# Kernel optimization log

Measured on AMD Instinct MI355X. Metric: run time of the kernel, lower is better.

Reference implementation:

```python
import jax, jax.numpy as jnp
import numpy as np

TAU = 2.0      # membrane time constant
V_TH = 1.0     # spike threshold (v_reset = 0, hard reset)
T_STEPS = 4    # num_steps

@jax.custom_vjp
def heaviside_atan(x):
    # forward: Heaviside; backward: spikingjelly ATan surrogate (alpha=2)
    return (x >= 0.0).astype(x.dtype)

def _h_fwd(x):
    return heaviside_atan(x), x

def _h_bwd(x, g):
    alpha = 2.0
    return (g * (alpha / 2.0) / (1.0 + (jnp.pi / 2.0 * alpha * x) ** 2),)

heaviside_atan.defvjp(_h_fwd, _h_bwd)

def lif_multistep(x_seq):
    # spikingjelly LIFNode, step_mode='m', decay_input=True, v_reset=0, detach_reset=True
    def step(v, x):
        v = v + (x - v) / TAU                      # charge
        s = heaviside_atan(v - V_TH)               # fire (surrogate grad)
        v = v * (1.0 - jax.lax.stop_gradient(s))   # hard reset, detached spike
        return v, s
    v0 = jnp.zeros_like(x_seq[0])
    _, spikes = jax.lax.scan(step, v0, x_seq)
    return spikes

def setup_inputs() -> dict:
    key = jax.random.key(0)
    k0, k1, k2 = jax.random.split(key, 3)
    B, L, C, D, NL = 16, 512, 128, 1024, 2
    inputs = jax.random.normal(k0, (B, L, C), jnp.float32)
    enc_W = jax.random.normal(k1, (C, D), jnp.float32) / np.sqrt(C).astype(np.float32)
    enc_b = jnp.zeros((D,), jnp.float32)
    W_cells = jax.random.normal(k2, (NL, D, D), jnp.float32) / np.sqrt(D).astype(np.float32)
    b_cells = jnp.zeros((NL, D), jnp.float32)
    return {"inputs": inputs, "enc_W": enc_W, "enc_b": enc_b,
            "W_cells": W_cells, "b_cells": b_cells}

def reference(inputs, enc_W, enc_b, W_cells, b_cells):
    # temporal spike encoder: repeat input over T steps, LIF-encode to spikes
    x = jnp.swapaxes(inputs, 1, 2)                       # [B, C, L]
    x = jnp.broadcast_to(x[None], (T_STEPS,) + x.shape)  # [T, B, C, L]
    h = lif_multistep(x)
    h = jnp.swapaxes(h, -2, -1)                          # [T, B, L, C]
    # encoder linear + init LIF
    h = lif_multistep(h @ enc_W + enc_b)                 # [T, B, L, D]
    # stacked SpikeRNNCells: Linear(D,D) -> multistep LIF
    for i in range(W_cells.shape[0]):
        h = lif_multistep(h @ W_cells[i] + b_cells[i])
    out = h.mean(0)                                      # [B, L, D]
    return out, out.mean(axis=1)                         # ([B,L,D], [B,D])
```

## Files before the change

### kernel.cpp

```cpp
#include <hip/hip_runtime.h>
#include <hip/hip_bf16.h>
#include <stdint.h>

#define TSTEPS 4

typedef __bf16 bf16_t;
typedef __attribute__((ext_vector_type(8))) __bf16 bf16x8;
typedef __attribute__((ext_vector_type(16))) float f32x16;
typedef __attribute__((ext_vector_type(4))) unsigned short ushort4v;

union frag_u { bf16x8 v; uint32_t d[4]; unsigned short u[8]; };

#define WT_VM2_LG0  0x072
#define WT_VM2      0xF72
#define WT_LG0      0xC07F
#define WT_VM0_LG0  0x070


__global__ void spike_encode_i8(const float* __restrict__ x,
                                uint4* __restrict__ s1)
{
    const int C = 128;
    int tid = blockIdx.x * blockDim.x + threadIdx.x;
    int row = tid & 31;
    int kb  = (tid >> 5) & 7;
    int m_blk = tid >> 8;
    int m = m_blk * 32 + row;
    const float* px = x + (size_t)m * C + kb * 16;
    float xv[16];
#pragma unroll
    for (int j = 0; j < 16; j += 4) {
        float4 t4 = *(const float4*)(px + j);
        xv[j] = t4.x; xv[j+1] = t4.y; xv[j+2] = t4.z; xv[j+3] = t4.w;
    }
    float v[16];
#pragma unroll
    for (int j = 0; j < 16; ++j) v[j] = 0.0f;
#pragma unroll
    for (int t = 0; t < TSTEPS; ++t) {
        uint32_t dw[4] = {0u, 0u, 0u, 0u};
#pragma unroll
        for (int j = 0; j < 16; ++j) {
            float vv = __fadd_rn(v[j], __fmul_rn(__fsub_rn(xv[j], v[j]), 0.5f));
            bool sp = (vv >= 1.0f);
            dw[j >> 2] |= sp ? (0x3Fu << ((j & 3) * 8)) : 0u;
            v[j] = sp ? 0.0f : vv;
        }
        uint4 o; o.x = dw[0]; o.y = dw[1]; o.z = dw[2]; o.w = dw[3];
        s1[((size_t)(m_blk * 8 + kb) * 4 + t) * 32 + row] = o;
    }
}

__global__ void split_transpose_all(const float* __restrict__ enc_W,
                                    const float* __restrict__ W_cells,
                                    bf16_t* __restrict__ W1h, bf16_t* __restrict__ W1l,
                                    bf16_t* __restrict__ W2h, bf16_t* __restrict__ W2l,
                                    bf16_t* __restrict__ W3h, bf16_t* __restrict__ W3l)
{
    const int N = 1024;
    const float* W;
    bf16_t *hi, *lo;
    int K;
    if (blockIdx.z == 0) {
        if (blockIdx.x >= 4) return;
        W = enc_W; hi = W1h; lo = W1l; K = 128;
    } else if (blockIdx.z == 1) {
        W = W_cells; hi = W2h; lo = W2l; K = 1024;
    } else {
        W = W_cells + (size_t)1024 * 1024; hi = W3h; lo = W3l; K = 1024;
    }
    const int NKB = K >> 4;
    __shared__ float tile[32][33];
    int k0 = blockIdx.x * 32, n0 = blockIdx.y * 32;
    int tx = threadIdx.x & 31, ty = threadIdx.x >> 5;
    for (int kk = ty; kk < 32; kk += 8)
        tile[kk][tx] = W[(size_t)(k0 + kk) * N + n0 + tx];
    __syncthreads();

    const int nn = tx;
    const int oc = ty;
    const int o2 = oc & 3;
    const bool isLo = (oc >> 2) != 0;
    const int kblk = (k0 >> 4) + (o2 >> 1);
    const int lane_in_packet = nn + 32 * (o2 & 1);

    frag_u f;
#pragma unroll
    for (int j = 0; j < 8; ++j) {
        float wv = tile[o2 * 8 + j][nn];
        bf16_t h = (bf16_t)wv;
        bf16_t l = (bf16_t)(wv - (float)h);
        f.v[j] = isLo ? (bf16_t)(2.0f * (float)l)
                      : (bf16_t)(2.0f * (float)h);
    }
    bf16_t* dst = (isLo ? lo : hi)
        + ((size_t)((n0 + nn) >> 5) * NKB + kblk) * 512 + lane_in_packet * 8;
    *(bf16x8*)dst = f.v;
}

template <int K, bool LAST>
__global__ __launch_bounds__(256, 4)
void gemm_lif_mfma(const uint8_t* __restrict__ Abytes,
                   const bf16_t* __restrict__ Bh,
                   const bf16_t* __restrict__ Bl,
                   const float* __restrict__ bias,
                   uint8_t* __restrict__ Sbytes,
                   float* __restrict__ Out,
                   int M, int N)
{
    constexpr int NKB = K >> 4;
    __shared__ __align__(16) uint8_t ldsR[4][8192];
    __shared__ __align__(8) unsigned short sh[4][256];

    const int tid = threadIdx.x;
    const int lane = tid & 63;
    const int wid = tid >> 6;
    const int l31 = lane & 31;
    const int half = lane >> 5;

    const int bid = blockIdx.x;
    const int xcd = bid & 7;
    const int j   = bid >> 3;
    const int nh   = j >> 7;
    const int r    = j & 127;
    const int mloc = r >> 3;
    const int n_t  = nh * 8 + (r & 7);
    const int m_t  = xcd * 16 + mloc;

    const int m0 = m_t * 64, n0 = n_t * 64;
    const int wave_m = (wid & 1) * 32;
    const int wave_n = (wid >> 1) * 32;
    const int m_blk = (m0 + wave_m) >> 5;

    const uint8_t* src0;
    const uint8_t* src1;
    int sstride, d0off, d1off;
    if (wid < 2) {
        const uint8_t* base = Abytes + ((size_t)(m0 >> 5) + wid) * NKB * 2048;
        src0 = base + (lane << 4);
        src1 = base + 1024 + (lane << 4);
        sstride = 2048;
        d0off = wid * 2048;
        d1off = d0off + 1024;
    } else {
        const int nl = wid - 2;
        src0 = (const uint8_t*)(Bh + ((size_t)(n0 >> 5) + nl) * NKB * 512)
               + (lane << 4);
        src1 = (const uint8_t*)(Bl + ((size_t)(n0 >> 5) + nl) * NKB * 512)
               + (lane << 4);
        sstride = 1024;
        d0off = 4096 + nl * 2048;
        d1off = d0off + 1024;
    }
    uint8_t* ringBase = &ldsR[0][0];

    const int aRdOff = (wid & 1) * 2048 + l31 * 16 + half * 8;
    const int bRdOff = 4096 + ((wid >> 1) << 11) + (lane << 4);

    f32x16 acc[TSTEPS];
#pragma unroll
    for (int t = 0; t < TSTEPS; ++t)
        for (int rr = 0; rr < 16; ++rr) acc[t][rr] = 0.0f;

    uint2 fm[4];
    bf16x8 cfh, cfl;

#define STAGE2(kb_) {                                                         \
    __builtin_amdgcn_global_load_lds(                                         \
        (const __attribute__((address_space(1))) uint32_t*)                   \
            (src0 + (size_t)(kb_) * sstride),                                 \
        (__attribute__((address_space(3))) uint32_t*)                         \
            (ringBase + (((kb_) & 3) << 13) + d0off),                         \
        16, 0, 0);                                                            \
    __builtin_amdgcn_global_load_lds(                                         \
        (const __attribute__((address_space(1))) uint32_t*)                   \
            (src1 + (size_t)(kb_) * sstride),                                 \
        (__attribute__((address_space(3))) uint32_t*)                         \
            (ringBase + (((kb_) & 3) << 13) + d1off),                         \
        16, 0, 0);                                                            \
    }

#define FRAGRD(kb_) {                                                        \
        const uint8_t* sb = ringBase + (((kb_) & 3) << 13);                  \
        fm[0] = *(const uint2*)(sb + aRdOff);                                \
        fm[1] = *(const uint2*)(sb + aRdOff + 512);                          \
        fm[2] = *(const uint2*)(sb + aRdOff + 1024);                         \
        fm[3] = *(const uint2*)(sb + aRdOff + 1536);                         \
        cfh = *(const bf16x8*)(sb + bRdOff);                                 \
        cfl = *(const bf16x8*)(sb + bRdOff + 1024);                          \
    }

#define EXPANDF(a_, f_) {                                                    \
        (f_).d[0] = __builtin_amdgcn_perm((a_).x, 0u, 0x05000400u);          \
        (f_).d[1] = __builtin_amdgcn_perm((a_).x, 0u, 0x07000600u);          \
        (f_).d[2] = __builtin_amdgcn_perm((a_).y, 0u, 0x05000400u);          \
        (f_).d[3] = __builtin_amdgcn_perm((a_).y, 0u, 0x07000600u);          \
    }

#define MFMAS() {                                                            \
        frag_u af0, af1, af2, af3;                                           \
        EXPANDF(fm[0], af0);                                                 \
        EXPANDF(fm[1], af1);                                                 \
        EXPANDF(fm[2], af2);                                                 \
        EXPANDF(fm[3], af3);                                                 \
        acc[0] = __builtin_amdgcn_mfma_f32_32x32x16_bf16(af0.v, cfh, acc[0], 0, 0, 0); \
        acc[1] = __builtin_amdgcn_mfma_f32_32x32x16_bf16(af1.v, cfh, acc[1], 0, 0, 0); \
        acc[2] = __builtin_amdgcn_mfma_f32_32x32x16_bf16(af2.v, cfh, acc[2], 0, 0, 0); \
        acc[3] = __builtin_amdgcn_mfma_f32_32x32x16_bf16(af3.v, cfh, acc[3], 0, 0, 0); \
        acc[0] = __builtin_amdgcn_mfma_f32_32x32x16_bf16(af0.v, cfl, acc[0], 0, 0, 0); \
        acc[1] = __builtin_amdgcn_mfma_f32_32x32x16_bf16(af1.v, cfl, acc[1], 0, 0, 0); \
        acc[2] = __builtin_amdgcn_mfma_f32_32x32x16_bf16(af2.v, cfl, acc[2], 0, 0, 0); \
        acc[3] = __builtin_amdgcn_mfma_f32_32x32x16_bf16(af3.v, cfl, acc[3], 0, 0, 0); \
    }

    STAGE2(0);
    STAGE2(1);
    __builtin_amdgcn_s_waitcnt(WT_VM2);
    asm volatile("" ::: "memory");
    __builtin_amdgcn_s_barrier();
    asm volatile("" ::: "memory");
    FRAGRD(0);

    for (int kb = 0; kb < NKB - 2; ++kb) {
        STAGE2(kb + 2);
        __builtin_amdgcn_s_waitcnt(WT_VM2_LG0);
        asm volatile("" ::: "memory");
        MFMAS();
        __builtin_amdgcn_s_barrier();
        asm volatile("" ::: "memory");
        FRAGRD(kb + 1);
    }
    __builtin_amdgcn_s_waitcnt(WT_VM0_LG0);
    asm volatile("" ::: "memory");
    MFMAS();
    __builtin_amdgcn_s_barrier();
    asm volatile("" ::: "memory");
    FRAGRD(NKB - 1);
    __builtin_amdgcn_s_waitcnt(WT_LG0);
    asm volatile("" ::: "memory");
    MFMAS();

#undef MFMAS
#undef EXPANDF
#undef FRAGRD
#undef STAGE2

    const float bv = bias[n0 + wave_n + l31];
    f32x16 vmem;
#pragma unroll
    for (int rr = 0; rr < 16; ++rr) vmem[rr] = 0.0f;
    uint64_t bits = 0ull;
    unsigned short* myt = &sh[wid][0];

    const int NKBo = N >> 4;
    const int kbase = (n0 + wave_n) >> 4;

    for (int t = 0; t < TSTEPS; ++t) {
#pragma unroll
        for (int rr = 0; rr < 16; ++rr) {
            float y = __fadd_rn(acc[t][rr], bv);
            float vv = vmem[rr];
            vv = __fadd_rn(vv, __fmul_rn(__fsub_rn(y, vv), 0.5f));
            bool sp = (vv >= 1.0f);
            vmem[rr] = sp ? 0.0f : vv;
            if (LAST) {
                bits |= sp ? (1ull << (rr * 4 + t)) : 0ull;
            } else {
                unsigned long long b = __ballot(sp);
                if (l31 == 0) {
                    uint32_t hb = (uint32_t)(b >> (half * 32));
                    int rowi = (rr & 3) + 8 * (rr >> 2) + 4 * half;
                    myt[(rowi * 2 + 0) * 4 + t] = (unsigned short)hb;
                    myt[(rowi * 2 + 1) * 4 + t] = (unsigned short)(hb >> 16);
                }
            }
        }
    }

    if (LAST) {
        float psum = 0.0f;
#pragma unroll
        for (int rr = 0; rr < 16; ++rr) {
            int m_r = (rr & 3) + 8 * (rr >> 2) + 4 * half;
            int m = m0 + wave_m + m_r;
            int n = n0 + wave_n + l31;
            int cnt = __popc((unsigned)((bits >> (rr * 4)) & 0xFull));
            float val = 0.25f * (float)cnt;
            Out[(size_t)m * N + n] = val;
            psum += val;
        }
        psum += __shfl_xor(psum, 32, 64);
        if (half == 0) {
            float* out2 = Out + (size_t)M * N;
            int b = m0 >> 9;
            int n = n0 + wave_n + l31;
            atomicAdd(out2 + (size_t)b * N + n, psum * (1.0f / 512.0f));
        }
    } else {
        const ushort4v pk = *(const ushort4v*)&myt[(l31 * 2 + half) * 4];
#pragma unroll
        for (int t = 0; t < TSTEPS; ++t) {
            uint32_t m16 = pk[t];
            uint4 o;
            o.x = (((m16      ) & 0xFu) * 0x00204081u & 0x01010101u) * 0x3Fu;
            o.y = (((m16 >>  4) & 0xFu) * 0x00204081u & 0x01010101u) * 0x3Fu;
            o.z = (((m16 >>  8) & 0xFu) * 0x00204081u & 0x01010101u) * 0x3Fu;
            o.w = (((m16 >> 12) & 0xFu) * 0x00204081u & 0x01010101u) * 0x3Fu;
            *(uint4*)(Sbytes + ((((size_t)m_blk * NKBo + kbase + half) * 4 + t)
                                * 32 + l31) * 16) = o;
        }
    }
}

__global__ void zero_out2(float* __restrict__ out2, int n)
{
    int i = blockIdx.x * blockDim.x + threadIdx.x;
    if (i < n) out2[i] = 0.0f;
}

extern "C" void kernel_launch(void* const* d_in, const int* in_sizes, int n_in,
                              void* d_out, int out_size, void* d_ws, size_t ws_size,
                              hipStream_t stream)
{
    const float* inputs  = (const float*)d_in[0];
    const float* enc_W   = (const float*)d_in[1];
    const float* enc_b   = (const float*)d_in[2];
    const float* W_cells = (const float*)d_in[3];
    const float* b_cells = (const float*)d_in[4];

    const int B = 16, L = 512, C = 128, D = 1024;
    const int M = B * L;

    char* ws = (char*)d_ws;
    size_t off = 0;
    uint8_t* s1 = (uint8_t*)(ws + off);
    off += (size_t)(M / 32) * (C / 16) * 4 * 32 * 16;
    bf16_t* W1h = (bf16_t*)(ws + off); off += (size_t)C * D * 2;
    bf16_t* W1l = (bf16_t*)(ws + off); off += (size_t)C * D * 2;
    bf16_t* W2h = (bf16_t*)(ws + off); off += (size_t)D * D * 2;
    bf16_t* W2l = (bf16_t*)(ws + off); off += (size_t)D * D * 2;
    bf16_t* W3h = (bf16_t*)(ws + off); off += (size_t)D * D * 2;
    bf16_t* W3l = (bf16_t*)(ws + off); off += (size_t)D * D * 2;
    uint8_t* h0 = (uint8_t*)(ws + off);
    off += (size_t)(M / 32) * (D / 16) * 4 * 32 * 16;
    uint8_t* h1 = (uint8_t*)(ws + off);

    float* out  = (float*)d_out;
    float* out2 = out + (size_t)M * D;

    split_transpose_all<<<dim3(32, 32, 3), 256, 0, stream>>>(
        enc_W, W_cells, W1h, W1l, W2h, W2l, W3h, W3l);

    spike_encode_i8<<<256, 256, 0, stream>>>(inputs, (uint4*)s1);

    zero_out2<<<(B * D + 255) / 256, 256, 0, stream>>>(out2, B * D);

    const int nblocks = (M / 64) * (D / 64);
    gemm_lif_mfma<128, false><<<nblocks, 256, 0, stream>>>(
        s1, W1h, W1l, enc_b, h0, nullptr, M, D);
    gemm_lif_mfma<1024, false><<<nblocks, 256, 0, stream>>>(
        h0, W2h, W2l, b_cells, h1, nullptr, M, D);
    gemm_lif_mfma<1024, true><<<nblocks, 256, 0, stream>>>(
        h1, W3h, W3l, b_cells + D, nullptr, out, M, D);
}
```

Measured before the change: 279.3 us.

## Store spike activations as bf16 in global memory, dropping in-loop byte expansion

Spike activations were stored as packed bytes and expanded to bf16 fragments with perm instructions inside the GEMM main loop. They are now written as ready-to-use bf16 fragments, so the GEMM reads A fragments straight from LDS with no expansion. This removes the per-iteration ALU work but doubles A-side global traffic and LDS footprint: the slab grows to 12 KB, which limits occupancy, and the staging now issues three async loads per wave. The spike-encoder buffer is aliased onto h1 to save workspace.

```diff
diff --git a/kernel.cpp b/kernel.cpp
--- a/kernel.cpp
+++ b/kernel.cpp
@@ -11,14 +11,14 @@
 
 union frag_u { bf16x8 v; uint32_t d[4]; unsigned short u[8]; };
 
-#define WT_VM2_LG0  0x072
-#define WT_VM2      0xF72
+#define WT_VM3_LG0  0x073
+#define WT_VM3      0xF73
 #define WT_LG0      0xC07F
 #define WT_VM0_LG0  0x070
 
 
-__global__ void spike_encode_i8(const float* __restrict__ x,
-                                uint4* __restrict__ s1)
+__global__ void spike_encode_bf16(const float* __restrict__ x,
+                                  uint8_t* __restrict__ s1)
 {
     const int C = 128;
     int tid = blockIdx.x * blockDim.x + threadIdx.x;
@@ -36,18 +36,27 @@
     float v[16];
 #pragma unroll
     for (int j = 0; j < 16; ++j) v[j] = 0.0f;
+    uint8_t* pkt0 = s1 + (size_t)(m_blk * 8 + kb) * 4096;
 #pragma unroll
     for (int t = 0; t < TSTEPS; ++t) {
-        uint32_t dw[4] = {0u, 0u, 0u, 0u};
+        uint32_t m16 = 0u;
 #pragma unroll
         for (int j = 0; j < 16; ++j) {
             float vv = __fadd_rn(v[j], __fmul_rn(__fsub_rn(xv[j], v[j]), 0.5f));
             bool sp = (vv >= 1.0f);
-            dw[j >> 2] |= sp ? (0x3Fu << ((j & 3) * 8)) : 0u;
+            m16 |= sp ? (1u << j) : 0u;
             v[j] = sp ? 0.0f : vv;
         }
-        uint4 o; o.x = dw[0]; o.y = dw[1]; o.z = dw[2]; o.w = dw[3];
-        s1[((size_t)(m_blk * 8 + kb) * 4 + t) * 32 + row] = o;
+        uint32_t d[8];
+#pragma unroll
+        for (int jj = 0; jj < 8; ++jj) {
+            uint32_t x2 = (m16 >> (2 * jj)) & 3u;
+            d[jj] = ((x2 | (x2 << 15)) & 0x00010001u) * 0x3F00u;
+        }
+        uint4 o0; o0.x = d[0]; o0.y = d[1]; o0.z = d[2]; o0.w = d[3];
+        uint4 o1; o1.x = d[4]; o1.y = d[5]; o1.z = d[6]; o1.w = d[7];
+        *(uint4*)(pkt0 + (size_t)t * 1024 + row * 16)       = o0;
+        *(uint4*)(pkt0 + (size_t)t * 1024 + 512 + row * 16) = o1;
     }
 }
 
@@ -109,7 +118,8 @@
                    int M, int N)
 {
     constexpr int NKB = K >> 4;
-    __shared__ __align__(16) uint8_t ldsR[4][8192];
+    constexpr int SLAB = 12288;
+    __shared__ __align__(16) uint8_t ldsR[4][SLAB];
     __shared__ __align__(8) unsigned short sh[4][256];
 
     const int tid = threadIdx.x;
@@ -132,118 +142,100 @@
     const int wave_n = (wid >> 1) * 32;
     const int m_blk = (m0 + wave_m) >> 5;
 
-    const uint8_t* src0;
-    const uint8_t* src1;
-    int sstride, d0off, d1off;
-    if (wid < 2) {
-        const uint8_t* base = Abytes + ((size_t)(m0 >> 5) + wid) * NKB * 2048;
-        src0 = base + (lane << 4);
-        src1 = base + 1024 + (lane << 4);
-        sstride = 2048;
-        d0off = wid * 2048;
-        d1off = d0off + 1024;
-    } else {
-        const int nl = wid - 2;
-        src0 = (const uint8_t*)(Bh + ((size_t)(n0 >> 5) + nl) * NKB * 512)
-               + (lane << 4);
-        src1 = (const uint8_t*)(Bl + ((size_t)(n0 >> 5) + nl) * NKB * 512)
-               + (lane << 4);
-        sstride = 1024;
-        d0off = 4096 + nl * 2048;
-        d1off = d0off + 1024;
+    const uint8_t* csrc[3];
+    uint32_t cstride[3], cdst[3];
+#pragma unroll
+    for (int i = 0; i < 3; ++i) {
+        int c = wid * 3 + i;
+        if (c < 8) {
+            int ml = c >> 2, tt = c & 3;
+            csrc[i] = Abytes + ((size_t)((m0 >> 5) + ml)) * NKB * 4096
+                      + tt * 1024 + (lane << 4);
+            cstride[i] = 4096;
+            cdst[i] = ml * 4096 + tt * 1024;
+        } else {
+            int cb = c - 8, nl = cb >> 1, pl = cb & 1;
+            csrc[i] = (const uint8_t*)(pl ? Bl : Bh)
+                      + ((size_t)((n0 >> 5) + nl)) * NKB * 1024 + (lane << 4);
+            cstride[i] = 1024;
+            cdst[i] = 8192 + nl * 2048 + pl * 1024;
+        }
     }
     uint8_t* ringBase = &ldsR[0][0];
 
-    const int aRdOff = (wid & 1) * 2048 + l31 * 16 + half * 8;
-    const int bRdOff = 4096 + ((wid >> 1) << 11) + (lane << 4);
+    const int aRdOff = (wid & 1) * 4096 + half * 512 + l31 * 16;
+    const int bRdOff = 8192 + ((wid >> 1) << 11) + (lane << 4);
 
     f32x16 acc[TSTEPS];
 #pragma unroll
     for (int t = 0; t < TSTEPS; ++t)
         for (int rr = 0; rr < 16; ++rr) acc[t][rr] = 0.0f;
 
-    uint2 fm[4];
-    bf16x8 cfh, cfl;
-
-#define STAGE2(kb_) {                                                         \
-    __builtin_amdgcn_global_load_lds(                                         \
-        (const __attribute__((address_space(1))) uint32_t*)                   \
-            (src0 + (size_t)(kb_) * sstride),                                 \
-        (__attribute__((address_space(3))) uint32_t*)                         \
-            (ringBase + (((kb_) & 3) << 13) + d0off),                         \
-        16, 0, 0);                                                            \
-    __builtin_amdgcn_global_load_lds(                                         \
-        (const __attribute__((address_space(1))) uint32_t*)                   \
-            (src1 + (size_t)(kb_) * sstride),                                 \
-        (__attribute__((address_space(3))) uint32_t*)                         \
-            (ringBase + (((kb_) & 3) << 13) + d1off),                         \
-        16, 0, 0);                                                            \
-    }
-
-#define FRAGRD(kb_) {                                                        \
-        const uint8_t* sb = ringBase + (((kb_) & 3) << 13);                  \
-        fm[0] = *(const uint2*)(sb + aRdOff);                                \
-        fm[1] = *(const uint2*)(sb + aRdOff + 512);                          \
-        fm[2] = *(const uint2*)(sb + aRdOff + 1024);                         \
-        fm[3] = *(const uint2*)(sb + aRdOff + 1536);                         \
+    bf16x8 af0, af1, af2, af3, cfh, cfl;
+
+#define STAGE3(kb_, sl_) {                                                    \
+    _Pragma("unroll")                                                         \
+    for (int i = 0; i < 3; ++i) {                                             \
+        __builtin_amdgcn_global_load_lds(                                     \
+            (const __attribute__((address_space(1))) uint32_t*)               \
+                (csrc[i] + (size_t)(kb_) * cstride[i]),                       \
+            (__attribute__((address_space(3))) uint32_t*)                     \
+                (ringBase + (sl_) * SLAB + cdst[i]),                          \
+            16, 0, 0);                                                        \
+    }                                                                         \
+    }
+
+#define FRAGRD(sl_) {                                                        \
+        const uint8_t* sb = ringBase + (sl_) * SLAB;                         \
+        af0 = *(const bf16x8*)(sb + aRdOff);                                 \
+        af1 = *(const bf16x8*)(sb + aRdOff + 1024);                          \
+        af2 = *(const bf16x8*)(sb + aRdOff + 2048);                          \
+        af3 = *(const bf16x8*)(sb + aRdOff + 3072);                          \
         cfh = *(const bf16x8*)(sb + bRdOff);                                 \
         cfl = *(const bf16x8*)(sb + bRdOff + 1024);                          \
     }
 
-#define EXPANDF(a_, f_) {                                                    \
-        (f_).d[0] = __builtin_amdgcn_perm((a_).x, 0u, 0x05000400u);          \
-        (f_).d[1] = __builtin_amdgcn_perm((a_).x, 0u, 0x07000600u);          \
-        (f_).d[2] = __builtin_amdgcn_perm((a_).y, 0u, 0x05000400u);          \
-        (f_).d[3] = __builtin_amdgcn_perm((a_).y, 0u, 0x07000600u);          \
-    }
-
 #define MFMAS() {                                                            \
-        frag_u af0, af1, af2, af3;                                           \
-        EXPANDF(fm[0], af0);                                                 \
-        EXPANDF(fm[1], af1);                                                 \
-        EXPANDF(fm[2], af2);                                                 \
-        EXPANDF(fm[3], af3);                                                 \
-        acc[0] = __builtin_amdgcn_mfma_f32_32x32x16_bf16(af0.v, cfh, acc[0], 0, 0, 0); \
-        acc[1] = __builtin_amdgcn_mfma_f32_32x32x16_bf16(af1.v, cfh, acc[1], 0, 0, 0); \
-        acc[2] = __builtin_amdgcn_mfma_f32_32x32x16_bf16(af2.v, cfh, acc[2], 0, 0, 0); \
-        acc[3] = __builtin_amdgcn_mfma_f32_32x32x16_bf16(af3.v, cfh, acc[3], 0, 0, 0); \
-        acc[0] = __builtin_amdgcn_mfma_f32_32x32x16_bf16(af0.v, cfl, acc[0], 0, 0, 0); \
-        acc[1] = __builtin_amdgcn_mfma_f32_32x32x16_bf16(af1.v, cfl, acc[1], 0, 0, 0); \
-        acc[2] = __builtin_amdgcn_mfma_f32_32x32x16_bf16(af2.v, cfl, acc[2], 0, 0, 0); \
-        acc[3] = __builtin_amdgcn_mfma_f32_32x32x16_bf16(af3.v, cfl, acc[3], 0, 0, 0); \
-    }
-
-    STAGE2(0);
-    STAGE2(1);
-    __builtin_amdgcn_s_waitcnt(WT_VM2);
+        acc[0] = __builtin_amdgcn_mfma_f32_32x32x16_bf16(af0, cfh, acc[0], 0, 0, 0); \
+        acc[1] = __builtin_amdgcn_mfma_f32_32x32x16_bf16(af1, cfh, acc[1], 0, 0, 0); \
+        acc[2] = __builtin_amdgcn_mfma_f32_32x32x16_bf16(af2, cfh, acc[2], 0, 0, 0); \
+        acc[3] = __builtin_amdgcn_mfma_f32_32x32x16_bf16(af3, cfh, acc[3], 0, 0, 0); \
+        acc[0] = __builtin_amdgcn_mfma_f32_32x32x16_bf16(af0, cfl, acc[0], 0, 0, 0); \
+        acc[1] = __builtin_amdgcn_mfma_f32_32x32x16_bf16(af1, cfl, acc[1], 0, 0, 0); \
+        acc[2] = __builtin_amdgcn_mfma_f32_32x32x16_bf16(af2, cfl, acc[2], 0, 0, 0); \
+        acc[3] = __builtin_amdgcn_mfma_f32_32x32x16_bf16(af3, cfl, acc[3], 0, 0, 0); \
+    }
+
+    STAGE3(0, 0);
+    STAGE3(1, 1);
+    __builtin_amdgcn_s_waitcnt(WT_VM3);
     asm volatile("" ::: "memory");
     __builtin_amdgcn_s_barrier();
     asm volatile("" ::: "memory");
     FRAGRD(0);
 
     for (int kb = 0; kb < NKB - 2; ++kb) {
-        STAGE2(kb + 2);
-        __builtin_amdgcn_s_waitcnt(WT_VM2_LG0);
+        STAGE3(kb + 2, (kb + 2) & 3);
+        __builtin_amdgcn_s_waitcnt(WT_VM3_LG0);
         asm volatile("" ::: "memory");
         MFMAS();
         __builtin_amdgcn_s_barrier();
         asm volatile("" ::: "memory");
-        FRAGRD(kb + 1);
+        FRAGRD((kb + 1) & 3);
     }
     __builtin_amdgcn_s_waitcnt(WT_VM0_LG0);
     asm volatile("" ::: "memory");
     MFMAS();
     __builtin_amdgcn_s_barrier();
     asm volatile("" ::: "memory");
-    FRAGRD(NKB - 1);
+    FRAGRD((NKB - 1) & 3);
     __builtin_amdgcn_s_waitcnt(WT_LG0);
     asm volatile("" ::: "memory");
     MFMAS();
 
 #undef MFMAS
-#undef EXPANDF
 #undef FRAGRD
-#undef STAGE2
+#undef STAGE3
 
     const float bv = bias[n0 + wave_n + l31];
     f32x16 vmem;
@@ -298,16 +290,21 @@
         }
     } else {
         const ushort4v pk = *(const ushort4v*)&myt[(l31 * 2 + half) * 4];
+        uint8_t* pkt0 = Sbytes
+            + ((size_t)m_blk * NKBo + kbase + half) * 4096;
 #pragma unroll
         for (int t = 0; t < TSTEPS; ++t) {
             uint32_t m16 = pk[t];
-            uint4 o;
-            o.x = (((m16      ) & 0xFu) * 0x00204081u & 0x01010101u) * 0x3Fu;
-            o.y = (((m16 >>  4) & 0xFu) * 0x00204081u & 0x01010101u) * 0x3Fu;
-            o.z = (((m16 >>  8) & 0xFu) * 0x00204081u & 0x01010101u) * 0x3Fu;
-            o.w = (((m16 >> 12) & 0xFu) * 0x00204081u & 0x01010101u) * 0x3Fu;
-            *(uint4*)(Sbytes + ((((size_t)m_blk * NKBo + kbase + half) * 4 + t)
-                                * 32 + l31) * 16) = o;
+            uint32_t d[8];
+#pragma unroll
+            for (int jj = 0; jj < 8; ++jj) {
+                uint32_t x2 = (m16 >> (2 * jj)) & 3u;
+                d[jj] = ((x2 | (x2 << 15)) & 0x00010001u) * 0x3F00u;
+            }
+            uint4 o0; o0.x = d[0]; o0.y = d[1]; o0.z = d[2]; o0.w = d[3];
+            uint4 o1; o1.x = d[4]; o1.y = d[5]; o1.z = d[6]; o1.w = d[7];
+            *(uint4*)(pkt0 + (size_t)t * 1024 + l31 * 16)       = o0;
+            *(uint4*)(pkt0 + (size_t)t * 1024 + 512 + l31 * 16) = o1;
         }
     }
 }
@@ -333,8 +330,6 @@
 
     char* ws = (char*)d_ws;
     size_t off = 0;
-    uint8_t* s1 = (uint8_t*)(ws + off);
-    off += (size_t)(M / 32) * (C / 16) * 4 * 32 * 16;
     bf16_t* W1h = (bf16_t*)(ws + off); off += (size_t)C * D * 2;
     bf16_t* W1l = (bf16_t*)(ws + off); off += (size_t)C * D * 2;
     bf16_t* W2h = (bf16_t*)(ws + off); off += (size_t)D * D * 2;
@@ -342,8 +337,9 @@
     bf16_t* W3h = (bf16_t*)(ws + off); off += (size_t)D * D * 2;
     bf16_t* W3l = (bf16_t*)(ws + off); off += (size_t)D * D * 2;
     uint8_t* h0 = (uint8_t*)(ws + off);
-    off += (size_t)(M / 32) * (D / 16) * 4 * 32 * 16;
+    off += (size_t)(M / 32) * (D / 16) * 4096;
     uint8_t* h1 = (uint8_t*)(ws + off);
+    uint8_t* s1 = h1;
 
     float* out  = (float*)d_out;
     float* out2 = out + (size_t)M * D;
@@ -351,7 +347,7 @@
     split_transpose_all<<<dim3(32, 32, 3), 256, 0, stream>>>(
         enc_W, W_cells, W1h, W1l, W2h, W2l, W3h, W3l);
 
-    spike_encode_i8<<<256, 256, 0, stream>>>(inputs, (uint4*)s1);
+    spike_encode_bf16<<<256, 256, 0, stream>>>(inputs, s1);
 
     zero_out2<<<(B * D + 255) / 256, 256, 0, stream>>>(out2, B * D);
 
```

New measurement: 309.1 us. 10.7% more time.
